# Kernel tuning notes

Hardware: AMD Instinct MI355X
Metric: run time of the kernel (lower is better)

## Reference

```python
import jax, jax.numpy as jnp
import numpy as np

B, C = 16384, 2048
DELTA_REL = 0.1


def setup_inputs() -> dict:
    key = jax.random.key(0)
    k1, k2, k3 = jax.random.split(key, 3)
    logits = jax.random.normal(k1, (B, C), dtype=jnp.float32)
    u = jax.random.uniform(k2, (B, C), dtype=jnp.float32)
    lab = (jax.random.uniform(k3, (B, C)) > 0.7).astype(jnp.float32)
    targets = jnp.where(u < 0.4, jnp.float32(jnp.nan), lab)
    return {"logits": logits, "targets": targets, "epoch": 3}


def _large_loss_rejection(logits, targets, epoch):
    unknown = jnp.isnan(targets)
    # unknown_to_negative: NaN -> 0 (negative label)
    t = jnp.where(unknown, 0.0, targets)
    # stable BCE-with-logits: softplus(x) - x*t
    losses = jax.nn.softplus(logits) - logits * t

    # --- no-grad mask construction ---
    ul = jax.lax.stop_gradient(losses) * unknown.astype(losses.dtype)
    percent = jnp.minimum(epoch * DELTA_REL, 1.0).astype(jnp.float32)
    n_unknown = jnp.count_nonzero(ul)
    k = jnp.round(n_unknown.astype(jnp.float32) * percent).astype(jnp.int32)
    k = jnp.maximum(k, 1)
    # k-th largest value of flattened unknown losses = topk(k).values.min()
    sorted_desc = jnp.sort(ul.reshape(-1))[::-1]
    loss_threshold = jax.lax.dynamic_slice(sorted_desc, (k - 1,), (1,))[0]
    lambdas = jnp.where(ul > loss_threshold, 0.0, 1.0)

    return losses * lambdas  # reduction='none'


def reference(logits, targets, epoch):
    return _large_loss_rejection(logits, targets, epoch)
```

## Files before the change

### kernel.cpp

```cpp
#include <hip/hip_runtime.h>
#include <math.h>

#define HC_OFF     0u
#define H12_OFF    16384u
#define H64_OFF    20480u
#define CTRL_OFF   20544u
#define ZERO_WORDS 20560u

#define FLOOR_BITS 0x36000000u

__device__ __forceinline__ float softplus_exact(float x) {
    float ax = fabsf(x);
    float e = (float)exp(-(double)ax);
    float l = (float)log1p((double)e);
    return fmaxf(x, 0.0f) + l;
}
__device__ __forceinline__ unsigned exact_bits(float x) {
    return __float_as_uint(softplus_exact(x));
}

__device__ __forceinline__ unsigned refine_A(float x, float* spo) {
    float ax = fabsf(x);
    float e = __expf(-ax);
    float sp = fmaxf(x, 0.0f) + __logf(1.0f + e);
    unsigned cb = __float_as_uint(sp);
    float mf = 64.0f + 8.0f * ax;
    if (x < 0.0f) mf += __builtin_amdgcn_rcpf(e);
    bool need = (cb < FLOOR_BITS) || (mf >= 524288.0f);
    if (!need) {
        unsigned m = (unsigned)mf;
        unsigned low = cb & 0xFFFFFu;
        need = (low < m) || (low >= 0x100000u - m);
    }
    if (need) {
        sp = softplus_exact(x);
        cb = __float_as_uint(sp);
    }
    *spo = sp;
    return cb;
}

__global__ __launch_bounds__(256) void kA_store_hist(
    const float* __restrict__ lg, const float* __restrict__ tg,
    float* __restrict__ out, unsigned* __restrict__ ws, long long n) {
    __shared__ unsigned sh[2][4096];
    for (int i = threadIdx.x; i < 4096; i += 256) { sh[0][i] = 0; sh[1][i] = 0; }
    __syncthreads();
    int hsel = threadIdx.x & 1;

    long long n4 = n >> 2;
    long long tid = (long long)blockIdx.x * 256 + threadIdx.x;
    long long stride = (long long)gridDim.x * 256;
    const float4* lg4 = (const float4*)lg;
    const float4* tg4 = (const float4*)tg;
    float4* out4 = (float4*)out;

    for (long long i = tid; i < n4; i += stride) {
        float4 x4 = lg4[i];
        float4 t4 = tg4[i];
        float xs[4] = {x4.x, x4.y, x4.z, x4.w};
        float ts[4] = {t4.x, t4.y, t4.z, t4.w};
        float os[4];
#pragma unroll
        for (int c = 0; c < 4; ++c) {
            float x = xs[c], t = ts[c];
            if (isnan(t)) {
                float sp;
                unsigned cb = refine_A(x, &sp);
                if (cb != 0u) atomicAdd(&sh[hsel][cb >> 20], 1u);
                os[c] = sp;
            } else {
                float ax = fabsf(x);
                float sp = fmaxf(x, 0.0f) + __logf(1.0f + __expf(-ax));
                float loss = sp - x * t;
                os[c] = __uint_as_float(__float_as_uint(loss) ^ 0x80000000u);
            }
        }
        float4 o = {os[0], os[1], os[2], os[3]};
        out4[i] = o;
    }
    if (tid == 0) {
        for (long long i = (n4 << 2); i < n; ++i) {
            float x = lg[i], t = tg[i];
            if (isnan(t)) {
                float sp;
                unsigned cb = refine_A(x, &sp);
                if (cb != 0u) atomicAdd(&sh[0][cb >> 20], 1u);
                out[i] = sp;
            } else {
                float sp = fmaxf(x, 0.0f) + __logf(1.0f + __expf(-fabsf(x)));
                float loss = sp - x * t;
                out[i] = __uint_as_float(__float_as_uint(loss) ^ 0x80000000u);
            }
        }
    }
    __syncthreads();
    unsigned* hist12 = ws + H12_OFF;
    for (int i = threadIdx.x; i < 4096; i += 256) {
        unsigned v = sh[0][i] + sh[1][i];
        if (v) atomicAdd(&hist12[i], v);
    }
}

__global__ __launch_bounds__(256) void k2_sel12(
    unsigned* __restrict__ ws, const int* __restrict__ epoch_ptr) {
    const unsigned* hist12 = ws + H12_OFF;
    unsigned* ctrl = ws + CTRL_OFF;
    __shared__ unsigned long long chunk[256];
    int t = threadIdx.x;
    unsigned long long s = 0;
    for (int j = 0; j < 16; ++j) s += hist12[t * 16 + j];
    chunk[t] = s;
    __syncthreads();
    if (t == 0) {
        unsigned long long tot = 0;
        for (int c = 0; c < 256; ++c) tot += chunk[c];
        int epoch = epoch_ptr[0];
        float percent = fminf((float)epoch * 0.1f, 1.0f);
        float nf = (float)tot;
        float kr = rintf(nf * percent);
        long long k = (long long)kr;
        if (k < 1) k = 1;

        long long cum = 0;
        int b = -1;
        long long kprime = 0;
        for (int c = 255; c >= 0; --c) {
            if (cum + (long long)chunk[c] >= k) {
                long long cc = cum;
                for (int j = 15; j >= 0; --j) {
                    unsigned v = hist12[c * 16 + j];
                    if (cc + (long long)v >= k) {
                        b = c * 16 + j;
                        kprime = k - cc;
                        break;
                    }
                    cc += v;
                }
                break;
            }
            cum += chunk[c];
        }
        ctrl[0] = (unsigned)b;
        ctrl[1] = (unsigned)kprime;
        if (b < 0) {
            ctrl[2] = 0u;
            ctrl[4] = 0xFFFFFFFFu;
            ctrl[6] = 0u;
        } else {
            unsigned lo12 = (unsigned)b << 20;
            double vlo = (double)__uint_as_float(lo12);
            double vhi = (double)__uint_as_float(lo12 + 0xFFFFFu);
            double mb = 1e9;
            if (vlo > 1e-30) {
                double xlo = vlo + log1p(-exp(-vlo)) - 0.001;
                double xhi = vhi + log1p(-exp(-vhi)) + 0.001;
                double axmax = fmax(fabs(xlo), fabs(xhi));
                mb = 64.0 + 8.0 * ceil(axmax);
                if (xlo < 0.0) mb += exp(fmin(-xlo, 30.0));
                mb *= 2.0;
            }
            ctrl[6] = (mb >= 8192.0) ? 8192u : (unsigned)mb;
        }
    }
}

__global__ __launch_bounds__(256) void kB_hist64(
    const float* __restrict__ lg, const unsigned* __restrict__ ob,
    unsigned* __restrict__ ws, long long n) {
    unsigned b12 = ws[CTRL_OFF + 0];
    if (b12 == 0xFFFFFFFFu) return;
    unsigned lo12 = b12 << 20;
    unsigned hi12 = lo12 + (1u << 20);
    unsigned m = ws[CTRL_OFF + 6];

    __shared__ unsigned sh[64];
    if (threadIdx.x < 64) sh[threadIdx.x] = 0;
    __syncthreads();

    long long n4 = n >> 2;
    long long tid = (long long)blockIdx.x * 256 + threadIdx.x;
    long long stride = (long long)gridDim.x * 256;
    const uint4* o4 = (const uint4*)ob;

    for (long long i = tid; i < n4; i += stride) {
        uint4 u4 = o4[i];
        unsigned us[4] = {u4.x, u4.y, u4.z, u4.w};
#pragma unroll
        for (int c = 0; c < 4; ++c) {
            unsigned u = us[c];
            if (u != 0u && u >= lo12 && u < hi12) {
                unsigned rB = u;
                unsigned d = u & 16383u;
                if (d < m || d >= 16384u - m)
                    rB = exact_bits(lg[i * 4 + c]);
                atomicAdd(&sh[(rB >> 14) & 63u], 1u);
            }
        }
    }
    if (tid == 0) {
        for (long long i = (n4 << 2); i < n; ++i) {
            unsigned u = ob[i];
            if (u != 0u && u >= lo12 && u < hi12) {
                unsigned rB = u;
                unsigned d = u & 16383u;
                if (d < m || d >= 16384u - m) rB = exact_bits(lg[i]);
                atomicAdd(&sh[(rB >> 14) & 63u], 1u);
            }
        }
    }
    __syncthreads();
    if (threadIdx.x < 64 && sh[threadIdx.x])
        atomicAdd(&ws[H64_OFF + threadIdx.x], sh[threadIdx.x]);
}

__global__ void k4_sel64(unsigned* __restrict__ ws) {
    unsigned* ctrl = ws + CTRL_OFF;
    if (ctrl[0] == 0xFFFFFFFFu) return;
    if (threadIdx.x == 0) {
        long long kprime = (long long)ctrl[1];
        long long cum = 0;
        int s = 0;
        long long kpp = 1;
        for (int j = 63; j >= 0; --j) {
            unsigned v = ws[H64_OFF + j];
            if (cum + (long long)v >= kprime) {
                s = j;
                kpp = kprime - cum;
                break;
            }
            cum += v;
        }
        ctrl[4] = (ctrl[0] << 20) + ((unsigned)s << 14);
        ctrl[5] = (unsigned)kpp;
    }
}

__global__ __launch_bounds__(256) void kC_histwin(
    const float* __restrict__ lg, const unsigned* __restrict__ ob,
    unsigned* __restrict__ ws, long long n) {
    unsigned wlo = ws[CTRL_OFF + 4];
    if (wlo == 0xFFFFFFFFu) return;
    unsigned whi = wlo + 16384u;
    unsigned m = ws[CTRL_OFF + 6];
    unsigned b12 = ws[CTRL_OFF + 0];
    unsigned lo12 = b12 << 20;
    unsigned hi12 = lo12 + (1u << 20);
    unsigned glo = (wlo - lo12 > m) ? wlo - m : lo12;
    unsigned ghi = (hi12 - whi > m) ? whi + m : hi12;

    long long n4 = n >> 2;
    long long tid = (long long)blockIdx.x * 256 + threadIdx.x;
    long long stride = (long long)gridDim.x * 256;
    const uint4* o4 = (const uint4*)ob;

    for (long long i = tid; i < n4; i += stride) {
        uint4 u4 = o4[i];
        unsigned us[4] = {u4.x, u4.y, u4.z, u4.w};
#pragma unroll
        for (int c = 0; c < 4; ++c) {
            unsigned u = us[c];
            if (u != 0u && u >= glo && u < ghi) {
                float x = lg[i * 4 + c];
                unsigned eb = exact_bits(x);
                unsigned rB = u;
                unsigned d = u & 16383u;
                if (d < m || d >= 16384u - m) rB = eb;
                if (rB >= wlo && rB < whi) {
                    unsigned off = eb - wlo;
                    if (off < 16384u) atomicAdd(&ws[HC_OFF + off], 1u);
                }
            }
        }
    }
    if (tid == 0) {
        for (long long i = (n4 << 2); i < n; ++i) {
            unsigned u = ob[i];
            if (u != 0u && u >= glo && u < ghi) {
                unsigned eb = exact_bits(lg[i]);
                unsigned rB = u;
                unsigned d = u & 16383u;
                if (d < m || d >= 16384u - m) rB = eb;
                if (rB >= wlo && rB < whi) {
                    unsigned off = eb - wlo;
                    if (off < 16384u) atomicAdd(&ws[HC_OFF + off], 1u);
                }
            }
        }
    }
}

__global__ __launch_bounds__(1024) void k6_selwin(unsigned* __restrict__ ws) {
    unsigned* ctrl = ws + CTRL_OFF;
    if (ctrl[4] == 0xFFFFFFFFu) return;
    __shared__ unsigned long long csum[1024];
    int t = threadIdx.x;
    unsigned long long s = 0;
    for (int j = 0; j < 16; ++j) s += ws[HC_OFF + t * 16 + j];
    csum[t] = s;
    __syncthreads();
    if (t == 0) {
        long long kpp = (long long)ctrl[5];
        long long cum = 0;
        int sel = 0;
        long long rem = kpp;
        for (int c = 1023; c >= 0; --c) {
            if (cum + (long long)csum[c] >= kpp) {
                sel = c;
                rem = kpp - cum;
                break;
            }
            cum += csum[c];
        }
        long long cc = 0;
        int bsel = 0;
        for (int j = 15; j >= 0; --j) {
            unsigned v = ws[HC_OFF + sel * 16 + j];
            if (cc + (long long)v >= rem) {
                bsel = j;
                break;
            }
            cc += v;
        }
        ctrl[2] = ctrl[4] + (unsigned)(sel * 16 + bsel);
    }
}

__global__ __launch_bounds__(256) void kD_final(
    const float* __restrict__ lg, unsigned* __restrict__ ob,
    const unsigned* __restrict__ ws, long long n) {
    unsigned thr = ws[CTRL_OFF + 2];
    unsigned m = ws[CTRL_OFF + 6];

    long long n4 = n >> 2;
    long long tid = (long long)blockIdx.x * 256 + threadIdx.x;
    long long stride = (long long)gridDim.x * 256;
    uint4* o4 = (uint4*)ob;

    for (long long i = tid; i < n4; i += stride) {
        uint4 u4 = o4[i];
        unsigned us[4] = {u4.x, u4.y, u4.z, u4.w};
        unsigned vs[4];
#pragma unroll
        for (int c = 0; c < 4; ++c) {
            unsigned u = us[c];
            if (u & 0x80000000u) {
                vs[c] = u ^ 0x80000000u;
            } else {
                unsigned udiff = (u > thr) ? u - thr : thr - u;
                if (udiff <= m) {
                    unsigned eb = exact_bits(lg[i * 4 + c]);
                    vs[c] = (eb > thr) ? 0u : eb;
                } else {
                    vs[c] = (u > thr) ? 0u : u;
                }
            }
        }
        uint4 v4 = {vs[0], vs[1], vs[2], vs[3]};
        o4[i] = v4;
    }
    if (tid == 0) {
        for (long long i = (n4 << 2); i < n; ++i) {
            unsigned u = ob[i];
            if (u & 0x80000000u) {
                ob[i] = u ^ 0x80000000u;
            } else {
                unsigned udiff = (u > thr) ? u - thr : thr - u;
                if (udiff <= m) {
                    unsigned eb = exact_bits(lg[i]);
                    ob[i] = (eb > thr) ? 0u : eb;
                } else {
                    ob[i] = (u > thr) ? 0u : u;
                }
            }
        }
    }
}

extern "C" void kernel_launch(void* const* d_in, const int* in_sizes, int n_in,
                              void* d_out, int out_size, void* d_ws, size_t ws_size,
                              hipStream_t stream) {
    const float* lg = (const float*)d_in[0];
    const float* tg = (const float*)d_in[1];
    const int* epoch = (const int*)d_in[2];
    float* out = (float*)d_out;
    unsigned* ob = (unsigned*)d_out;
    unsigned* ws = (unsigned*)d_ws;
    long long n = (long long)in_sizes[0];

    hipMemsetAsync(d_ws, 0, (size_t)ZERO_WORDS * 4, stream);

    const int blocks = 2048, threads = 256;
    kA_store_hist<<<blocks, threads, 0, stream>>>(lg, tg, out, ws, n);
    k2_sel12<<<1, 256, 0, stream>>>(ws, epoch);
    kB_hist64<<<blocks, threads, 0, stream>>>(lg, ob, ws, n);
    k4_sel64<<<1, 64, 0, stream>>>(ws);
    kC_histwin<<<blocks, threads, 0, stream>>>(lg, ob, ws, n);
    k6_selwin<<<1, 1024, 0, stream>>>(ws);
    kD_final<<<blocks, threads, 0, stream>>>(lg, ob, ws, n);
}
```

Before: 257.2 us.

## Compact threshold-bin candidates in hist64 pass so window histogram skips full scan

kB_hist64 now gathers the logits of every element in the selected 12-bit bin. Each block collects them in a shared-memory buffer and appends them to a global candidate list in the workspace. kC_histwin then recomputes bits from this short list instead of rescanning the whole output and logits arrays, with a fallback to the full scan if the list overflows. It also launches with fewer blocks. kA drops its duplicated shared histogram (used to reduce atomic contention) and stores the raw loss bits, which adds some extra atomic and global-write work in kB and may raise shared-atomic contention in kA.

```diff
diff --git a/kernel.cpp b/kernel.cpp
--- a/kernel.cpp
+++ b/kernel.cpp
@@ -6,6 +6,9 @@
 #define H64_OFF    20480u
 #define CTRL_OFF   20544u
 #define ZERO_WORDS 20560u
+#define CAND_OFF   20560u
+#define CAND_CAP   900000u
+#define LBUF       2048u
 
 #define FLOOR_BITS 0x36000000u
 
@@ -43,10 +46,9 @@
 __global__ __launch_bounds__(256) void kA_store_hist(
     const float* __restrict__ lg, const float* __restrict__ tg,
     float* __restrict__ out, unsigned* __restrict__ ws, long long n) {
-    __shared__ unsigned sh[2][4096];
-    for (int i = threadIdx.x; i < 4096; i += 256) { sh[0][i] = 0; sh[1][i] = 0; }
-    __syncthreads();
-    int hsel = threadIdx.x & 1;
+    __shared__ unsigned sh[4096];
+    for (int i = threadIdx.x; i < 4096; i += 256) sh[i] = 0;
+    __syncthreads();
 
     long long n4 = n >> 2;
     long long tid = (long long)blockIdx.x * 256 + threadIdx.x;
@@ -67,8 +69,8 @@
             if (isnan(t)) {
                 float sp;
                 unsigned cb = refine_A(x, &sp);
-                if (cb != 0u) atomicAdd(&sh[hsel][cb >> 20], 1u);
-                os[c] = sp;
+                if (cb != 0u) atomicAdd(&sh[cb >> 20], 1u);
+                os[c] = __uint_as_float(cb);
             } else {
                 float ax = fabsf(x);
                 float sp = fmaxf(x, 0.0f) + __logf(1.0f + __expf(-ax));
@@ -85,8 +87,8 @@
             if (isnan(t)) {
                 float sp;
                 unsigned cb = refine_A(x, &sp);
-                if (cb != 0u) atomicAdd(&sh[0][cb >> 20], 1u);
-                out[i] = sp;
+                if (cb != 0u) atomicAdd(&sh[0], 0u), atomicAdd(&sh[cb >> 20], 1u);
+                out[i] = __uint_as_float(cb);
             } else {
                 float sp = fmaxf(x, 0.0f) + __logf(1.0f + __expf(-fabsf(x)));
                 float loss = sp - x * t;
@@ -96,10 +98,8 @@
     }
     __syncthreads();
     unsigned* hist12 = ws + H12_OFF;
-    for (int i = threadIdx.x; i < 4096; i += 256) {
-        unsigned v = sh[0][i] + sh[1][i];
-        if (v) atomicAdd(&hist12[i], v);
-    }
+    for (int i = threadIdx.x; i < 4096; i += 256)
+        if (sh[i]) atomicAdd(&hist12[i], sh[i]);
 }
 
 __global__ __launch_bounds__(256) void k2_sel12(
@@ -175,8 +175,14 @@
     unsigned m = ws[CTRL_OFF + 6];
 
     __shared__ unsigned sh[64];
+    __shared__ float buf[LBUF];
+    __shared__ unsigned lcnt, gbase;
     if (threadIdx.x < 64) sh[threadIdx.x] = 0;
-    __syncthreads();
+    if (threadIdx.x == 0) lcnt = 0;
+    __syncthreads();
+
+    float* cand = (float*)(ws + CAND_OFF);
+    unsigned* cnt = ws + CTRL_OFF + 3;
 
     long long n4 = n >> 2;
     long long tid = (long long)blockIdx.x * 256 + threadIdx.x;
@@ -190,11 +196,14 @@
         for (int c = 0; c < 4; ++c) {
             unsigned u = us[c];
             if (u != 0u && u >= lo12 && u < hi12) {
+                float x = lg[i * 4 + c];
                 unsigned rB = u;
                 unsigned d = u & 16383u;
                 if (d < m || d >= 16384u - m)
-                    rB = exact_bits(lg[i * 4 + c]);
+                    rB = exact_bits(x);
                 atomicAdd(&sh[(rB >> 14) & 63u], 1u);
+                unsigned li = atomicAdd(&lcnt, 1u);
+                if (li < LBUF) buf[li] = x;
             }
         }
     }
@@ -202,16 +211,29 @@
         for (long long i = (n4 << 2); i < n; ++i) {
             unsigned u = ob[i];
             if (u != 0u && u >= lo12 && u < hi12) {
+                float x = lg[i];
                 unsigned rB = u;
                 unsigned d = u & 16383u;
-                if (d < m || d >= 16384u - m) rB = exact_bits(lg[i]);
+                if (d < m || d >= 16384u - m) rB = exact_bits(x);
                 atomicAdd(&sh[(rB >> 14) & 63u], 1u);
+                unsigned idx = atomicAdd(cnt, 1u);
+                if (idx < CAND_CAP) cand[idx] = x;
             }
         }
     }
     __syncthreads();
     if (threadIdx.x < 64 && sh[threadIdx.x])
         atomicAdd(&ws[H64_OFF + threadIdx.x], sh[threadIdx.x]);
+    if (threadIdx.x == 0) {
+        unsigned add = (lcnt > LBUF) ? (CAND_CAP + 1u) : lcnt;
+        gbase = atomicAdd(cnt, add);
+    }
+    __syncthreads();
+    unsigned c2 = lcnt < LBUF ? lcnt : LBUF;
+    for (unsigned j = threadIdx.x; j < c2; j += 256) {
+        unsigned gi = gbase + j;
+        if (gi < CAND_CAP) cand[gi] = buf[j];
+    }
 }
 
 __global__ void k4_sel64(unsigned* __restrict__ ws) {
@@ -248,20 +270,18 @@
     unsigned hi12 = lo12 + (1u << 20);
     unsigned glo = (wlo - lo12 > m) ? wlo - m : lo12;
     unsigned ghi = (hi12 - whi > m) ? whi + m : hi12;
-
-    long long n4 = n >> 2;
+    unsigned count = ws[CTRL_OFF + 3];
+
     long long tid = (long long)blockIdx.x * 256 + threadIdx.x;
     long long stride = (long long)gridDim.x * 256;
-    const uint4* o4 = (const uint4*)ob;
-
-    for (long long i = tid; i < n4; i += stride) {
-        uint4 u4 = o4[i];
-        unsigned us[4] = {u4.x, u4.y, u4.z, u4.w};
-#pragma unroll
-        for (int c = 0; c < 4; ++c) {
-            unsigned u = us[c];
-            if (u != 0u && u >= glo && u < ghi) {
-                float x = lg[i * 4 + c];
+
+    if (count <= CAND_CAP) {
+        const float* cand = (const float*)(ws + CAND_OFF);
+        for (long long i = tid; i < (long long)count; i += stride) {
+            float x = cand[i];
+            float spd;
+            unsigned u = refine_A(x, &spd);
+            if (u >= glo && u < ghi) {
                 unsigned eb = exact_bits(x);
                 unsigned rB = u;
                 unsigned d = u & 16383u;
@@ -272,18 +292,40 @@
                 }
             }
         }
-    }
-    if (tid == 0) {
-        for (long long i = (n4 << 2); i < n; ++i) {
-            unsigned u = ob[i];
-            if (u != 0u && u >= glo && u < ghi) {
-                unsigned eb = exact_bits(lg[i]);
-                unsigned rB = u;
-                unsigned d = u & 16383u;
-                if (d < m || d >= 16384u - m) rB = eb;
-                if (rB >= wlo && rB < whi) {
-                    unsigned off = eb - wlo;
-                    if (off < 16384u) atomicAdd(&ws[HC_OFF + off], 1u);
+    } else {
+        long long n4 = n >> 2;
+        const uint4* o4 = (const uint4*)ob;
+        for (long long i = tid; i < n4; i += stride) {
+            uint4 u4 = o4[i];
+            unsigned us[4] = {u4.x, u4.y, u4.z, u4.w};
+#pragma unroll
+            for (int c = 0; c < 4; ++c) {
+                unsigned u = us[c];
+                if (u != 0u && u >= glo && u < ghi) {
+                    float x = lg[i * 4 + c];
+                    unsigned eb = exact_bits(x);
+                    unsigned rB = u;
+                    unsigned d = u & 16383u;
+                    if (d < m || d >= 16384u - m) rB = eb;
+                    if (rB >= wlo && rB < whi) {
+                        unsigned off = eb - wlo;
+                        if (off < 16384u) atomicAdd(&ws[HC_OFF + off], 1u);
+                    }
+                }
+            }
+        }
+        if (tid == 0) {
+            for (long long i = (n4 << 2); i < n; ++i) {
+                unsigned u = ob[i];
+                if (u != 0u && u >= glo && u < ghi) {
+                    unsigned eb = exact_bits(lg[i]);
+                    unsigned rB = u;
+                    unsigned d = u & 16383u;
+                    if (d < m || d >= 16384u - m) rB = eb;
+                    if (rB >= wlo && rB < whi) {
+                        unsigned off = eb - wlo;
+                        if (off < 16384u) atomicAdd(&ws[HC_OFF + off], 1u);
+                    }
                 }
             }
         }
@@ -395,7 +437,7 @@
     k2_sel12<<<1, 256, 0, stream>>>(ws, epoch);
     kB_hist64<<<blocks, threads, 0, stream>>>(lg, ob, ws, n);
     k4_sel64<<<1, 64, 0, stream>>>(ws);
-    kC_histwin<<<blocks, threads, 0, stream>>>(lg, ob, ws, n);
+    kC_histwin<<<1024, threads, 0, stream>>>(lg, ob, ws, n);
     k6_selwin<<<1, 1024, 0, stream>>>(ws);
     kD_final<<<blocks, threads, 0, stream>>>(lg, ob, ws, n);
 }
```

Measured after the change: 265.5 us. +3.2%, slower.
